# Performance work log

Hardware: AMD Instinct MI355X
Metric: run time of the kernel (lower is better)

Reference implementation:

```python
import jax, jax.numpy as jnp
import numpy as np

B = 1024      # number of states
NP = 32       # SVGD particles per state
AD = 20       # act_dim
OD = 64       # obs_dim
H = 256       # critic hidden width
STEPS = 5     # num_svgd_steps
LR = 0.1      # svgd_lr (adaptive_lr disabled)
SP0 = 1.0     # svgd_sigma_p0
ALIM = 1.0    # act_limit


def _q(obs, X, w1, b1, w2, b2, w3, b3):
    h = jnp.concatenate([obs, X], axis=-1)
    h = jax.nn.relu(h @ w1 + b1)
    h = jax.nn.relu(h @ w2 + b2)
    return jnp.squeeze(h @ w3 + b3, -1)


def _rbf(X):
    # X: [B, NP, AD] -> K [B,NP,NP], diff [B,NP,NP,AD], gamma [B,1,1], K_grad [B,NP,NP,AD]
    diff = X[:, :, None, :] - X[:, None, :, :]
    dist_sq = jnp.sum(diff * diff, axis=-1)
    # adaptive bandwidth via median heuristic (adaptive_sig=True)
    med = jnp.median(dist_sq.reshape(dist_sq.shape[0], -1), axis=-1)
    sig_sq = med / (2.0 * jnp.log(NP + 1.0))
    gamma = (1.0 / (2.0 * sig_sq + 1e-8))[:, None, None]
    K = jnp.exp(-gamma * dist_sq)
    K_grad = -2.0 * gamma[..., None] * diff * K[..., None]  # d/dx_i K(x_i, x_j)
    return K, diff, gamma, K_grad


def setup_inputs():
    key = jax.random.key(0)
    ks = jax.random.split(key, 16)
    N = B * NP

    def lin(k, fi, fo):
        return (jax.random.normal(k, (fi, fo), jnp.float32) / np.sqrt(fi)).astype(jnp.float32)

    return {
        "obs": jax.random.normal(ks[0], (N, OD), jnp.float32),
        "a0": jax.random.normal(ks[1], (N, AD), jnp.float32) * np.sqrt(SP0),
        "q1_w1": lin(ks[2], OD + AD, H), "q1_b1": jnp.zeros((H,), jnp.float32),
        "q1_w2": lin(ks[3], H, H),       "q1_b2": jnp.zeros((H,), jnp.float32),
        "q1_w3": lin(ks[4], H, 1),       "q1_b3": jnp.zeros((1,), jnp.float32),
        "q2_w1": lin(ks[5], OD + AD, H), "q2_b1": jnp.zeros((H,), jnp.float32),
        "q2_w2": lin(ks[6], H, H),       "q2_b2": jnp.zeros((H,), jnp.float32),
        "q2_w3": lin(ks[7], H, 1),       "q2_b3": jnp.zeros((1,), jnp.float32),
    }


def reference(obs, a0, q1_w1, q1_b1, q1_w2, q1_b2, q1_w3, q1_b3,
              q2_w1, q2_b1, q2_w2, q2_b2, q2_w3, q2_b3):
    eye = jnp.eye(NP, dtype=a0.dtype)

    def q_min_sum(Xf):
        q1 = _q(obs, Xf, q1_w1, q1_b1, q1_w2, q1_b2, q1_w3, q1_b3)
        q2 = _q(obs, Xf, q2_w1, q2_b1, q2_w2, q2_b2, q2_w3, q2_b3)
        return jnp.sum(jnp.minimum(q1, q2))

    score_fn = jax.grad(q_min_sum)  # autograd score function

    def step(carry, _):
        a, logp = carry
        score = score_fn(a).reshape(-1, NP, AD)                 # [B,NP,AD]
        X = a.reshape(-1, NP, AD)
        K, diff, gamma, Kg = _rbf(X)
        phi = (jnp.einsum('bij,bjd->bid', K, score) + Kg.sum(axis=1)) / NP
        # log-prob correction terms (with_logprob=True)
        term1 = jnp.mean(jnp.sum(Kg * score[:, None, :, :], axis=-1), axis=2)     # [B,NP]
        inner = jnp.sum(jnp.transpose(Kg, (0, 2, 1, 3)) * diff, axis=-1) \
                - AD * (K - eye)
        term2 = -2.0 * gamma[:, :, 0] * jnp.mean(inner, axis=1)                   # [B,NP]
        logp = logp - LR * (term1 + term2)
        a = a + LR * phi.reshape(a.shape)                        # svgd_optim
        return (a, logp), None

    logp0 = jnp.zeros((B, NP), a0.dtype)
    (a, logp_svgd), _ = jax.lax.scan(step, (a0, logp0), None, length=STEPS)

    a_sq = ALIM * jnp.tanh(a)                                    # [B*NP, AD]
    logp_normal = (-AD * 0.5 * jnp.log(2.0 * jnp.pi * SP0)
                   - 0.5 / SP0 * jnp.sum(a0 * a0, axis=-1)).reshape(-1, NP)
    logp_tanh = -jnp.sum(2.0 * (jnp.log(2.0) - a - jax.nn.softplus(-2.0 * a)),
                         axis=-1).reshape(-1, NP)
    logp_a = jnp.mean(logp_normal + logp_svgd + logp_tanh, axis=-1)  # [B]
    return a_sq, logp_a
```

## Files before the change

kernel.cpp:

```cpp
#include <hip/hip_runtime.h>
#include <math.h>

#define NPART 32
#define ADIM  20
#define ODIM  64
#define HID   256
#define NSTEPS 5
#define LRC   0.1f
#define NBLK  512
#define LOG33 3.4965075614664802f

typedef short bf8 __attribute__((ext_vector_type(8)));
typedef float f4  __attribute__((ext_vector_type(4)));

#define OW1T(n) ((n)*24576)
#define OW2T(n) (49152 + (n)*65536)
#define OW2C(n) (180224 + (n)*65536)
#define OW1X(n) (311296 + (n)*8192)
#define OW3B(n) (327680 + (n)*256)
#define WS_ELEMS 328192

__device__ __forceinline__ short f2bf(float x) {
    unsigned u = __float_as_uint(x);
    u += 0x7FFFu + ((u >> 16) & 1u);
    return (short)(u >> 16);
}
__device__ __forceinline__ short f2bfT(float x) {
    return (short)(__float_as_uint(x) >> 16);
}
__device__ __forceinline__ float bf2f(short s) {
    return __uint_as_float(((unsigned)(unsigned short)s) << 16);
}

#define MFMA(a,b,c) __builtin_amdgcn_mfma_f32_16x16x32_bf16((a),(b),(c),0,0,0)

__global__ void prep_weights(const float* __restrict__ w1a, const float* __restrict__ w2a,
                             const float* __restrict__ w3a, const float* __restrict__ w1b,
                             const float* __restrict__ w2b, const float* __restrict__ w3b,
                             unsigned short* __restrict__ ws)
{
    int idx = blockIdx.x * 256 + threadIdx.x;
    if (idx >= WS_ELEMS) return;
    float val;
    if (idx < 49152) {
        int net = idx / 24576, rem = idx % 24576;
        int n = rem / 96, k = rem % 96;
        const float* w1 = net ? w1b : w1a;
        val = (k < 84) ? w1[k*256 + n] : 0.f;
    } else if (idx < 180224) {
        int t2 = idx - 49152; int net = t2 / 65536, rem = t2 % 65536;
        int n = rem / 256, k = rem % 256;
        const float* w2 = net ? w2b : w2a;
        val = w2[k*256 + n];
    } else if (idx < 311296) {
        int t2 = idx - 180224; int net = t2 / 65536, rem = t2 % 65536;
        const float* w2 = net ? w2b : w2a;
        val = w2[rem];
    } else if (idx < 327680) {
        int t2 = idx - 311296; int net = t2 / 8192, rem = t2 % 8192;
        int d = rem / 256, n = rem % 256;
        const float* w1 = net ? w1b : w1a;
        val = (d < 20) ? w1[(64 + d)*256 + n] : 0.f;
    } else {
        int t2 = idx - 327680; int net = t2 / 256, k = t2 % 256;
        const float* w3 = net ? w3b : w3a;
        val = w3[k];
    }
    ws[idx] = (unsigned short)f2bf(val);
}

__global__ void __launch_bounds__(512, 4)
svgd_main(const float* __restrict__ obs,  const float* __restrict__ a0g,
          const float* __restrict__ b1a,  const float* __restrict__ b2a, const float* __restrict__ b3a,
          const float* __restrict__ b1b,  const float* __restrict__ b2b, const float* __restrict__ b3b,
          const float* __restrict__ w3af, const float* __restrict__ w3bf,
          const unsigned short* __restrict__ ws, float* __restrict__ out)
{
    __shared__ __align__(16) short A0s[64*96];
    __shared__ __align__(16) short hbuf[64*264];
    __shared__ unsigned maskS[2][2][64][8];
    __shared__ float Xm[64*20];
    __shared__ float scoreS[64*21];
    __shared__ float qpart[2][8][64];
    __shared__ int   winsS[64];
    __shared__ float logps[64];
    __shared__ unsigned short lutI[496], lutJ[496];
    __shared__ float med2[4];
    __shared__ float qvS[64];
    __shared__ float normsS[64], diagS[64], rowKS[64];

    float* d2sF = (float*)hbuf;
    float* GSF  = ((float*)hbuf) + 2048;
    short* KbS  = hbuf + 8192;
    short* SBs  = hbuf + 10240;
    short* STbS = hbuf + 12288;
    short* XTbS = hbuf + 14336;

    const int t = threadIdx.x, b = blockIdx.x;
    const int lane = t & 63, wv = t >> 6;
    const int q = lane >> 4, mp = lane & 15;
    const int nb = wv * 32;

    for (int p = t; p < 64*ODIM; p += 512) {
        int i = p >> 6, d = p & 63;
        A0s[i*96 + d] = f2bfT(obs[(b*64 + i)*ODIM + d]);
    }
    for (int p = t; p < 64*ADIM; p += 512) {
        int i = p / 20, d = p - i*20;
        float v = a0g[(b*64 + i)*20 + d];
        Xm[p] = v;
        A0s[i*96 + 64 + d] = f2bfT(v);
    }
    for (int p = t; p < 64*12; p += 512) { int i = p/12, d = p - i*12; A0s[i*96 + 84 + d] = 0; }
    { unsigned* mz = &maskS[0][0][0][0];
      for (int p = t; p < 2*2*64*8; p += 512) mz[p] = 0u; }
    if (t < 496) {
        int i_ = 0, rem = t;
        while (rem >= 31 - i_) { rem -= 31 - i_; ++i_; }
        lutI[t] = (unsigned short)i_; lutJ[t] = (unsigned short)(i_ + 1 + rem);
    }
    if (t < 64) logps[t] = 0.f;
    __syncthreads();

    for (int step = 0; step < NSTEPS; ++step) {
        for (int net = 0; net < 2; ++net) {
            const unsigned short* w1t = ws + OW1T(net);
            const unsigned short* w2t = ws + OW2T(net);
            const float* b1p = net ? b1b : b1a;
            const float* b2p = net ? b2b : b2a;
            const float* w3p = net ? w3bf : w3af;

            f4 acc[4][2];
            #pragma unroll
            for (int h = 0; h < 4; ++h) { acc[h][0] = (f4){0,0,0,0}; acc[h][1] = (f4){0,0,0,0}; }
            {
                const unsigned short* bp0 = w1t + (size_t)(nb +      mp)*96 + q*8;
                const unsigned short* bp1 = w1t + (size_t)(nb + 16 + mp)*96 + q*8;
                bf8 bb0 = *(const bf8*)bp0, bb1 = *(const bf8*)bp1;
                #pragma unroll
                for (int k0 = 0; k0 < 96; k0 += 32) {
                    bf8 n0 = bb0, n1 = bb1;
                    if (k0 + 32 < 96) { n0 = *(const bf8*)(bp0 + k0 + 32); n1 = *(const bf8*)(bp1 + k0 + 32); }
                    #pragma unroll
                    for (int h = 0; h < 4; ++h) {
                        bf8 aa = *(const bf8*)&A0s[(h*16 + mp)*96 + k0 + q*8];
                        acc[h][0] = MFMA(aa, bb0, acc[h][0]);
                        acc[h][1] = MFMA(aa, bb1, acc[h][1]);
                    }
                    bb0 = n0; bb1 = n1;
                }
            }
            #pragma unroll
            for (int h = 0; h < 4; ++h) {
                #pragma unroll
                for (int s = 0; s < 2; ++s) {
                    int n0 = nb + s*16, col = n0 + mp;
                    float bias = b1p[col];
                    #pragma unroll
                    for (int r = 0; r < 4; ++r) {
                        float v = acc[h][s][r] + bias;
                        bool pos = v > 0.f;
                        unsigned long long bal = __ballot(pos);
                        hbuf[(h*16 + q*4 + r)*264 + col] = f2bfT(pos ? v : 0.f);
                        if (mp == 0)
                            atomicOr(&maskS[net][0][h*16 + q*4 + r][n0 >> 5],
                                     ((unsigned)((bal >> (q*16)) & 0xFFFFull)) << (n0 & 16));
                    }
                }
            }
            __syncthreads();

            #pragma unroll
            for (int h = 0; h < 4; ++h) { acc[h][0] = (f4){0,0,0,0}; acc[h][1] = (f4){0,0,0,0}; }
            {
                const unsigned short* bp0 = w2t + (size_t)(nb +      mp)*256 + q*8;
                const unsigned short* bp1 = w2t + (size_t)(nb + 16 + mp)*256 + q*8;
                bf8 bb0 = *(const bf8*)bp0, bb1 = *(const bf8*)bp1;
                #pragma unroll
                for (int k0 = 0; k0 < 256; k0 += 32) {
                    bf8 n0 = bb0, n1 = bb1;
                    if (k0 + 32 < 256) { n0 = *(const bf8*)(bp0 + k0 + 32); n1 = *(const bf8*)(bp1 + k0 + 32); }
                    #pragma unroll
                    for (int h = 0; h < 4; ++h) {
                        bf8 aa = *(const bf8*)&hbuf[(h*16 + mp)*264 + k0 + q*8];
                        acc[h][0] = MFMA(aa, bb0, acc[h][0]);
                        acc[h][1] = MFMA(aa, bb1, acc[h][1]);
                    }
                    bb0 = n0; bb1 = n1;
                }
            }
            {
                float qp[4][4] = {{0,0,0,0},{0,0,0,0},{0,0,0,0},{0,0,0,0}};
                #pragma unroll
                for (int h = 0; h < 4; ++h) {
                    #pragma unroll
                    for (int s = 0; s < 2; ++s) {
                        int n0 = nb + s*16, col = n0 + mp;
                        float bias = b2p[col], w3v = w3p[col];
                        #pragma unroll
                        for (int r = 0; r < 4; ++r) {
                            float v = acc[h][s][r] + bias;
                            bool pos = v > 0.f;
                            unsigned long long bal = __ballot(pos);
                            if (mp == 0)
                                atomicOr(&maskS[net][1][h*16 + q*4 + r][n0 >> 5],
                                         ((unsigned)((bal >> (q*16)) & 0xFFFFull)) << (n0 & 16));
                            qp[h][r] += pos ? v * w3v : 0.f;
                        }
                    }
                }
                #pragma unroll
                for (int d = 1; d < 16; d <<= 1)
                    #pragma unroll
                    for (int h = 0; h < 4; ++h)
                        #pragma unroll
                        for (int r = 0; r < 4; ++r)
                            qp[h][r] += __shfl_xor(qp[h][r], d, 64);
                if (mp == 0) {
                    #pragma unroll
                    for (int h = 0; h < 4; ++h)
                        #pragma unroll
                        for (int r = 0; r < 4; ++r)
                            qpart[net][wv][h*16 + q*4 + r] = qp[h][r];
                }
            }
            __syncthreads();
        }

        if (t < 64) {
            float q0 = b3a[0], q1 = b3b[0];
            #pragma unroll
            for (int w = 0; w < 8; ++w) { q0 += qpart[0][w][t]; q1 += qpart[1][w][t]; }
            winsS[t] = (q0 <= q1) ? 0 : 1;
        }
        __syncthreads();

        for (int net = 0; net < 2; ++net) {
            const unsigned short* w2c  = ws + OW2C(net);
            const unsigned short* w3b8 = ws + OW3B(net);

            f4 acc[4][2];
            #pragma unroll
            for (int h = 0; h < 4; ++h) { acc[h][0] = (f4){0,0,0,0}; acc[h][1] = (f4){0,0,0,0}; }
            int win[4];
            #pragma unroll
            for (int h = 0; h < 4; ++h) win[h] = (winsS[h*16 + mp] == net);
            {
                const unsigned short* bp0 = w2c + (size_t)(nb +      mp)*256 + q*8;
                const unsigned short* bp1 = w2c + (size_t)(nb + 16 + mp)*256 + q*8;
                bf8 bb0 = *(const bf8*)bp0, bb1 = *(const bf8*)bp1;
                #pragma unroll
                for (int k0 = 0; k0 < 256; k0 += 32) {
                    bf8 n0 = bb0, n1 = bb1;
                    if (k0 + 32 < 256) { n0 = *(const bf8*)(bp0 + k0 + 32); n1 = *(const bf8*)(bp1 + k0 + 32); }
                    bf8 w3v = *(const bf8*)(w3b8 + k0 + q*8);
                    #pragma unroll
                    for (int h = 0; h < 4; ++h) {
                        unsigned bits = win[h] ? ((maskS[net][1][h*16 + mp][k0 >> 5] >> (q*8)) & 0xFFu) : 0u;
                        bf8 aa;
                        #pragma unroll
                        for (int j = 0; j < 8; ++j)
                            aa[j] = ((bits >> j) & 1u) ? w3v[j] : (short)0;
                        acc[h][0] = MFMA(aa, bb0, acc[h][0]);
                        acc[h][1] = MFMA(aa, bb1, acc[h][1]);
                    }
                    bb0 = n0; bb1 = n1;
                }
            }
            #pragma unroll
            for (int h = 0; h < 4; ++h) {
                #pragma unroll
                for (int s = 0; s < 2; ++s) {
                    int col = nb + s*16 + mp;
                    #pragma unroll
                    for (int r = 0; r < 4; ++r) {
                        int row = h*16 + q*4 + r;
                        bool on = (maskS[net][0][row][col >> 5] >> (col & 31)) & 1u;
                        hbuf[row*264 + col] = f2bfT(on ? acc[h][s][r] : 0.f);
                    }
                }
            }
            __syncthreads();
            {
                int mt = wv & 3, ch = wv >> 2;
                const unsigned short* w1x = ws + OW1X(net);
                const unsigned short* bp  = w1x + (size_t)(ch*16 + mp)*256 + q*8;
                f4 sa = (f4){0,0,0,0};
                bf8 bx = *(const bf8*)bp;
                #pragma unroll
                for (int k0 = 0; k0 < 256; k0 += 32) {
                    bf8 nx = bx;
                    if (k0 + 32 < 256) nx = *(const bf8*)(bp + k0 + 32);
                    bf8 aa = *(const bf8*)&hbuf[(mt*16 + mp)*264 + k0 + q*8];
                    sa = MFMA(aa, bx, sa);
                    bx = nx;
                }
                int colD = ch*16 + mp;
                if (colD < 20) {
                    #pragma unroll
                    for (int r = 0; r < 4; ++r) {
                        int row = mt*16 + q*4 + r;
                        if (net == 0) scoreS[row*21 + colD]  = sa[r];
                        else          scoreS[row*21 + colD] += sa[r];
                    }
                }
            }
            __syncthreads();
        }

        if (t < 64) {
            int st = t >> 5;
            float nrm = 0.f, dg = 0.f;
            #pragma unroll
            for (int d = 0; d < 20; ++d) {
                float xb = bf2f(A0s[t*96 + 64 + d]);
                nrm += xb * xb;
                float sv = scoreS[t*21 + d];
                float xv = Xm[t*20 + d];
                dg += xv * sv;
                short sb = f2bfT(sv);
                SBs[t*32 + d] = sb;
                STbS[st*1024 + d*32 + (t & 31)] = sb;
                XTbS[st*1024 + d*32 + (t & 31)] = f2bfT(xv);
            }
            #pragma unroll
            for (int d = 20; d < 32; ++d) SBs[t*32 + d] = 0;
            normsS[t] = nrm;
            diagS[t]  = dg;
        }
        __syncthreads();

        {
            int stw = wv >> 2, mt = (wv >> 1) & 1, nt = wv & 1;
            bf8 aa  = *(const bf8*)&A0s[(stw*32 + mt*16 + mp)*96 + 64 + q*8];
            bf8 bbx = *(const bf8*)&A0s[(stw*32 + nt*16 + mp)*96 + 64 + q*8];
            bf8 bbs = *(const bf8*)&SBs[(stw*32 + nt*16 + mp)*32 + q*8];
            f4 gx = MFMA(aa, bbx, ((f4){0,0,0,0}));
            f4 gs = MFMA(aa, bbs, ((f4){0,0,0,0}));
            int jl = nt*16 + mp;
            float nj = normsS[stw*32 + jl];
            #pragma unroll
            for (int r = 0; r < 4; ++r) {
                int il = mt*16 + q*4 + r;
                d2sF[stw*1024 + il*32 + jl] = normsS[stw*32 + il] + nj - 2.f*gx[r];
                GSF [stw*1024 + il*32 + jl] = gs[r];
            }
        }
        __syncthreads();

        if (wv < 2) {
            const float* base = d2sF + wv*1024;
            float v[8];
            #pragma unroll
            for (int i = 0; i < 8; ++i) {
                int e = lane*8 + i;
                v[i] = (e < 496) ? base[lutI[e]*32 + lutJ[e]] : 3.4e38f;
            }
            for (int k = 2; k <= 512; k <<= 1) {
                for (int jj = k >> 1; jj >= 8; jj >>= 1) {
                    int lm = jj >> 3;
                    #pragma unroll
                    for (int i = 0; i < 8; ++i) {
                        float w = __shfl_xor(v[i], lm, 64);
                        int p = lane*8 + i;
                        bool takeMin = (((p & k) == 0) == ((p & jj) == 0));
                        v[i] = takeMin ? fminf(v[i], w) : fmaxf(v[i], w);
                    }
                }
                int jj0 = (k >> 1) < 4 ? (k >> 1) : 4;
                for (int jj = jj0; jj >= 1; jj >>= 1) {
                    #pragma unroll
                    for (int i = 0; i < 8; ++i) {
                        if ((i & jj) == 0) {
                            int i2 = i | jj;
                            int p = lane*8 + i;
                            bool up = ((p & k) == 0);
                            float x = v[i], y = v[i2];
                            float mn = fminf(x, y), mx = fmaxf(x, y);
                            v[i] = up ? mn : mx; v[i2] = up ? mx : mn;
                        }
                    }
                }
            }
            if (lane == 29) med2[wv*2 + 0] = v[7];
            if (lane == 30) med2[wv*2 + 1] = v[0];
        } else {
            unsigned* mz = &maskS[0][0][0][0];
            for (int p = t - 128; p < 2*2*64*8; p += 384) mz[p] = 0u;
        }
        __syncthreads();

        {
            int i = t >> 3, stw = i >> 5, il = i & 31, j0 = (t & 7) * 4;
            float medv = 0.5f * (med2[stw*2] + med2[stw*2 + 1]);
            float gam  = 1.f / (2.f * (medv / (2.f * LOG33)) + 1e-8f);
            float sK = 0.f, sKGS = 0.f, sKd2 = 0.f, sKdg = 0.f;
            #pragma unroll
            for (int jj = 0; jj < 4; ++jj) {
                int j = j0 + jj;
                float d2 = d2sF[stw*1024 + il*32 + j];
                float K  = expf(-gam * d2);
                KbS[stw*1024 + il*32 + j] = f2bfT(K);
                sK   += K;
                sKGS += K * GSF[stw*1024 + il*32 + j];
                sKd2 += K * d2;
                sKdg += K * diagS[stw*32 + j];
            }
            #pragma unroll
            for (int d = 1; d < 8; d <<= 1) {
                sK   += __shfl_xor(sK,   d, 64);
                sKGS += __shfl_xor(sKGS, d, 64);
                sKd2 += __shfl_xor(sKd2, d, 64);
                sKdg += __shfl_xor(sKdg, d, 64);
            }
            if ((t & 7) == 0) {
                rowKS[i] = sK;
                float sdots = sKGS - sKdg;
                float ssum  = -2.f*gam*sdots
                              - 2.f*gam*(2.f*gam*sKd2 - 20.f*(sK - 1.f));
                logps[i] -= LRC * (ssum * (1.f/32.f));
            }
        }
        __syncthreads();

        {
            int stw = wv >> 2, mt = (wv >> 1) & 1, nt = wv & 1;
            float medv = 0.5f * (med2[stw*2] + med2[stw*2 + 1]);
            float gam  = 1.f / (2.f * (medv / (2.f * LOG33)) + 1e-8f);
            bf8 aa  = *(const bf8*)&KbS [stw*1024 + (mt*16 + mp)*32 + q*8];
            bf8 b1v = *(const bf8*)&STbS[stw*1024 + (nt*16 + mp)*32 + q*8];
            bf8 b2v = *(const bf8*)&XTbS[stw*1024 + (nt*16 + mp)*32 + q*8];
            f4 ks = MFMA(aa, b1v, ((f4){0,0,0,0}));
            f4 kx = MFMA(aa, b2v, ((f4){0,0,0,0}));
            int dd = nt*16 + mp;
            if (dd < 20) {
                #pragma unroll
                for (int r = 0; r < 4; ++r) {
                    int gi = stw*32 + mt*16 + q*4 + r;
                    float xi  = Xm[gi*20 + dd];
                    float phi = (ks[r] + 2.f*gam*(xi*rowKS[gi] - kx[r])) * (1.f/32.f);
                    float nx  = xi + LRC * phi;
                    Xm[gi*20 + dd] = nx;
                    A0s[gi*96 + 64 + dd] = f2bfT(nx);
                }
            }
        }
        __syncthreads();
    }

    for (int p = t; p < 64*20; p += 512) {
        int i = p / 20, d = p - i*20;
        out[(b*64 + i)*20 + d] = tanhf(Xm[p]);
    }
    if (t < 64) {
        float lt = 0.f, s0 = 0.f;
        for (int d = 0; d < 20; ++d) {
            float a  = Xm[t*20 + d];
            float x  = -2.f * a;
            float sp = fmaxf(x, 0.f) + log1pf(expf(-fabsf(x)));
            lt -= 2.f * (0.69314718056f - a - sp);
            float v = a0g[(b*64 + t)*20 + d];
            s0 += v * v;
        }
        qvS[t] = -18.3787706641f - 0.5f*s0 + logps[t] + lt;
    }
    __syncthreads();
    if (t < 2) {
        float s = 0.f;
        for (int i = 0; i < 32; ++i) s += qvS[t*32 + i];
        out[1024*32*20 + b*2 + t] = s * (1.f/32.f);
    }
}

extern "C" void kernel_launch(void* const* d_in, const int* in_sizes, int n_in,
                              void* d_out, int out_size, void* d_ws, size_t ws_size,
                              hipStream_t stream) {
    unsigned short* ws = (unsigned short*)d_ws;
    prep_weights<<<(WS_ELEMS + 255)/256, 256, 0, stream>>>(
        (const float*)d_in[2],  (const float*)d_in[4],  (const float*)d_in[6],
        (const float*)d_in[8],  (const float*)d_in[10], (const float*)d_in[12], ws);
    svgd_main<<<NBLK, 512, 0, stream>>>(
        (const float*)d_in[0],  (const float*)d_in[1],
        (const float*)d_in[3],  (const float*)d_in[5],  (const float*)d_in[7],
        (const float*)d_in[9],  (const float*)d_in[11], (const float*)d_in[13],
        (const float*)d_in[6],  (const float*)d_in[12],
        ws, (float*)d_out);
}
```

Before: 497.5 us.

## Interleave twin-critic forward and backward GEMMs to cut barriers and serialization

Unrolls the two-network loops and interleaves independent work. Net-1 layer-1 runs alongside net-0 layer-2, and net-0's backward GEMM runs alongside net-1 layer-2. The winner mask is now applied at the hidden-gradient stage instead of zeroing the weight operand. Score is accumulated in registers and written straight to bf16 buffers, and the diagonal term is read from the GS Gram matrix instead of a separate dot product. This removes several __syncthreads and the scoreS buffer, at the cost of more live accumulators and register pressure, and backward GEMMs now run for both nets on every row.

```diff
diff --git a/kernel.cpp b/kernel.cpp
--- a/kernel.cpp
+++ b/kernel.cpp
@@ -80,14 +80,13 @@
     __shared__ __align__(16) short hbuf[64*264];
     __shared__ unsigned maskS[2][2][64][8];
     __shared__ float Xm[64*20];
-    __shared__ float scoreS[64*21];
     __shared__ float qpart[2][8][64];
     __shared__ int   winsS[64];
     __shared__ float logps[64];
     __shared__ unsigned short lutI[496], lutJ[496];
     __shared__ float med2[4];
     __shared__ float qvS[64];
-    __shared__ float normsS[64], diagS[64], rowKS[64];
+    __shared__ float normsS[64], rowKS[64];
 
     float* d2sF = (float*)hbuf;
     float* GSF  = ((float*)hbuf) + 2048;
@@ -123,31 +122,20 @@
     __syncthreads();
 
     for (int step = 0; step < NSTEPS; ++step) {
-        for (int net = 0; net < 2; ++net) {
-            const unsigned short* w1t = ws + OW1T(net);
-            const unsigned short* w2t = ws + OW2T(net);
-            const float* b1p = net ? b1b : b1a;
-            const float* b2p = net ? b2b : b2a;
-            const float* w3p = net ? w3bf : w3af;
-
+        {
+            const unsigned short* w1t = ws + OW1T(0);
             f4 acc[4][2];
             #pragma unroll
             for (int h = 0; h < 4; ++h) { acc[h][0] = (f4){0,0,0,0}; acc[h][1] = (f4){0,0,0,0}; }
-            {
-                const unsigned short* bp0 = w1t + (size_t)(nb +      mp)*96 + q*8;
-                const unsigned short* bp1 = w1t + (size_t)(nb + 16 + mp)*96 + q*8;
-                bf8 bb0 = *(const bf8*)bp0, bb1 = *(const bf8*)bp1;
-                #pragma unroll
-                for (int k0 = 0; k0 < 96; k0 += 32) {
-                    bf8 n0 = bb0, n1 = bb1;
-                    if (k0 + 32 < 96) { n0 = *(const bf8*)(bp0 + k0 + 32); n1 = *(const bf8*)(bp1 + k0 + 32); }
-                    #pragma unroll
-                    for (int h = 0; h < 4; ++h) {
-                        bf8 aa = *(const bf8*)&A0s[(h*16 + mp)*96 + k0 + q*8];
-                        acc[h][0] = MFMA(aa, bb0, acc[h][0]);
-                        acc[h][1] = MFMA(aa, bb1, acc[h][1]);
-                    }
-                    bb0 = n0; bb1 = n1;
+            #pragma unroll
+            for (int k0 = 0; k0 < 96; k0 += 32) {
+                bf8 bb0 = *(const bf8*)(w1t + (size_t)(nb +      mp)*96 + k0 + q*8);
+                bf8 bb1 = *(const bf8*)(w1t + (size_t)(nb + 16 + mp)*96 + k0 + q*8);
+                #pragma unroll
+                for (int h = 0; h < 4; ++h) {
+                    bf8 aa = *(const bf8*)&A0s[(h*16 + mp)*96 + k0 + q*8];
+                    acc[h][0] = MFMA(aa, bb0, acc[h][0]);
+                    acc[h][1] = MFMA(aa, bb1, acc[h][1]);
                 }
             }
             #pragma unroll
@@ -155,7 +143,7 @@
                 #pragma unroll
                 for (int s = 0; s < 2; ++s) {
                     int n0 = nb + s*16, col = n0 + mp;
-                    float bias = b1p[col];
+                    float bias = b1a[col];
                     #pragma unroll
                     for (int r = 0; r < 4; ++r) {
                         float v = acc[h][s][r] + bias;
@@ -163,69 +151,172 @@
                         unsigned long long bal = __ballot(pos);
                         hbuf[(h*16 + q*4 + r)*264 + col] = f2bfT(pos ? v : 0.f);
                         if (mp == 0)
-                            atomicOr(&maskS[net][0][h*16 + q*4 + r][n0 >> 5],
+                            atomicOr(&maskS[0][0][h*16 + q*4 + r][n0 >> 5],
                                      ((unsigned)((bal >> (q*16)) & 0xFFFFull)) << (n0 & 16));
                     }
                 }
             }
-            __syncthreads();
-
-            #pragma unroll
-            for (int h = 0; h < 4; ++h) { acc[h][0] = (f4){0,0,0,0}; acc[h][1] = (f4){0,0,0,0}; }
-            {
-                const unsigned short* bp0 = w2t + (size_t)(nb +      mp)*256 + q*8;
-                const unsigned short* bp1 = w2t + (size_t)(nb + 16 + mp)*256 + q*8;
-                bf8 bb0 = *(const bf8*)bp0, bb1 = *(const bf8*)bp1;
-                #pragma unroll
-                for (int k0 = 0; k0 < 256; k0 += 32) {
-                    bf8 n0 = bb0, n1 = bb1;
-                    if (k0 + 32 < 256) { n0 = *(const bf8*)(bp0 + k0 + 32); n1 = *(const bf8*)(bp1 + k0 + 32); }
+        }
+        __syncthreads();
+
+        f4 accL2[4][2], accL1[4][2];
+        #pragma unroll
+        for (int h = 0; h < 4; ++h) {
+            accL2[h][0] = (f4){0,0,0,0}; accL2[h][1] = (f4){0,0,0,0};
+            accL1[h][0] = (f4){0,0,0,0}; accL1[h][1] = (f4){0,0,0,0};
+        }
+        {
+            const unsigned short* w2t = ws + OW2T(0);
+            const unsigned short* w1t = ws + OW1T(1);
+            #pragma unroll
+            for (int k0 = 0; k0 < 256; k0 += 32) {
+                bf8 b20 = *(const bf8*)(w2t + (size_t)(nb +      mp)*256 + k0 + q*8);
+                bf8 b21 = *(const bf8*)(w2t + (size_t)(nb + 16 + mp)*256 + k0 + q*8);
+                #pragma unroll
+                for (int h = 0; h < 4; ++h) {
+                    bf8 aa = *(const bf8*)&hbuf[(h*16 + mp)*264 + k0 + q*8];
+                    accL2[h][0] = MFMA(aa, b20, accL2[h][0]);
+                    accL2[h][1] = MFMA(aa, b21, accL2[h][1]);
+                }
+                if (k0 < 96) {
+                    bf8 c0 = *(const bf8*)(w1t + (size_t)(nb +      mp)*96 + k0 + q*8);
+                    bf8 c1 = *(const bf8*)(w1t + (size_t)(nb + 16 + mp)*96 + k0 + q*8);
                     #pragma unroll
                     for (int h = 0; h < 4; ++h) {
-                        bf8 aa = *(const bf8*)&hbuf[(h*16 + mp)*264 + k0 + q*8];
-                        acc[h][0] = MFMA(aa, bb0, acc[h][0]);
-                        acc[h][1] = MFMA(aa, bb1, acc[h][1]);
+                        bf8 aa = *(const bf8*)&A0s[(h*16 + mp)*96 + k0 + q*8];
+                        accL1[h][0] = MFMA(aa, c0, accL1[h][0]);
+                        accL1[h][1] = MFMA(aa, c1, accL1[h][1]);
                     }
-                    bb0 = n0; bb1 = n1;
-                }
-            }
-            {
-                float qp[4][4] = {{0,0,0,0},{0,0,0,0},{0,0,0,0},{0,0,0,0}};
+                }
+            }
+        }
+        {
+            float qp[4][4] = {{0,0,0,0},{0,0,0,0},{0,0,0,0},{0,0,0,0}};
+            #pragma unroll
+            for (int h = 0; h < 4; ++h) {
+                #pragma unroll
+                for (int s = 0; s < 2; ++s) {
+                    int n0 = nb + s*16, col = n0 + mp;
+                    float bias = b2a[col], w3v = w3af[col];
+                    #pragma unroll
+                    for (int r = 0; r < 4; ++r) {
+                        float v = accL2[h][s][r] + bias;
+                        bool pos = v > 0.f;
+                        unsigned long long bal = __ballot(pos);
+                        if (mp == 0)
+                            atomicOr(&maskS[0][1][h*16 + q*4 + r][n0 >> 5],
+                                     ((unsigned)((bal >> (q*16)) & 0xFFFFull)) << (n0 & 16));
+                        qp[h][r] += pos ? v * w3v : 0.f;
+                    }
+                }
+            }
+            #pragma unroll
+            for (int d = 1; d < 16; d <<= 1)
+                #pragma unroll
+                for (int h = 0; h < 4; ++h)
+                    #pragma unroll
+                    for (int r = 0; r < 4; ++r)
+                        qp[h][r] += __shfl_xor(qp[h][r], d, 64);
+            if (mp == 0) {
+                #pragma unroll
+                for (int h = 0; h < 4; ++h)
+                    #pragma unroll
+                    for (int r = 0; r < 4; ++r)
+                        qpart[0][wv][h*16 + q*4 + r] = qp[h][r];
+            }
+        }
+        __syncthreads();
+        #pragma unroll
+        for (int h = 0; h < 4; ++h) {
+            #pragma unroll
+            for (int s = 0; s < 2; ++s) {
+                int n0 = nb + s*16, col = n0 + mp;
+                float bias = b1b[col];
+                #pragma unroll
+                for (int r = 0; r < 4; ++r) {
+                    float v = accL1[h][s][r] + bias;
+                    bool pos = v > 0.f;
+                    unsigned long long bal = __ballot(pos);
+                    hbuf[(h*16 + q*4 + r)*264 + col] = f2bfT(pos ? v : 0.f);
+                    if (mp == 0)
+                        atomicOr(&maskS[1][0][h*16 + q*4 + r][n0 >> 5],
+                                 ((unsigned)((bal >> (q*16)) & 0xFFFFull)) << (n0 & 16));
+                }
+            }
+        }
+        __syncthreads();
+
+        f4 accB0[4][2];
+        #pragma unroll
+        for (int h = 0; h < 4; ++h) {
+            accL2[h][0] = (f4){0,0,0,0}; accL2[h][1] = (f4){0,0,0,0};
+            accB0[h][0] = (f4){0,0,0,0}; accB0[h][1] = (f4){0,0,0,0};
+        }
+        {
+            const unsigned short* w2t  = ws + OW2T(1);
+            const unsigned short* w2c  = ws + OW2C(0);
+            const unsigned short* w3b8 = ws + OW3B(0);
+            #pragma unroll
+            for (int k0 = 0; k0 < 256; k0 += 32) {
+                bf8 b20 = *(const bf8*)(w2t + (size_t)(nb +      mp)*256 + k0 + q*8);
+                bf8 b21 = *(const bf8*)(w2t + (size_t)(nb + 16 + mp)*256 + k0 + q*8);
                 #pragma unroll
                 for (int h = 0; h < 4; ++h) {
-                    #pragma unroll
-                    for (int s = 0; s < 2; ++s) {
-                        int n0 = nb + s*16, col = n0 + mp;
-                        float bias = b2p[col], w3v = w3p[col];
-                        #pragma unroll
-                        for (int r = 0; r < 4; ++r) {
-                            float v = acc[h][s][r] + bias;
-                            bool pos = v > 0.f;
-                            unsigned long long bal = __ballot(pos);
-                            if (mp == 0)
-                                atomicOr(&maskS[net][1][h*16 + q*4 + r][n0 >> 5],
-                                         ((unsigned)((bal >> (q*16)) & 0xFFFFull)) << (n0 & 16));
-                            qp[h][r] += pos ? v * w3v : 0.f;
-                        }
+                    bf8 aa = *(const bf8*)&hbuf[(h*16 + mp)*264 + k0 + q*8];
+                    accL2[h][0] = MFMA(aa, b20, accL2[h][0]);
+                    accL2[h][1] = MFMA(aa, b21, accL2[h][1]);
+                }
+                bf8 c0 = *(const bf8*)(w2c + (size_t)(nb +      mp)*256 + k0 + q*8);
+                bf8 c1 = *(const bf8*)(w2c + (size_t)(nb + 16 + mp)*256 + k0 + q*8);
+                bf8 w3v = *(const bf8*)(w3b8 + k0 + q*8);
+                #pragma unroll
+                for (int h = 0; h < 4; ++h) {
+                    unsigned bits = (maskS[0][1][h*16 + mp][k0 >> 5] >> (q*8)) & 0xFFu;
+                    bf8 aa;
+                    #pragma unroll
+                    for (int j = 0; j < 8; ++j)
+                        aa[j] = ((bits >> j) & 1u) ? w3v[j] : (short)0;
+                    accB0[h][0] = MFMA(aa, c0, accB0[h][0]);
+                    accB0[h][1] = MFMA(aa, c1, accB0[h][1]);
+                }
+            }
+        }
+        {
+            float qp[4][4] = {{0,0,0,0},{0,0,0,0},{0,0,0,0},{0,0,0,0}};
+            #pragma unroll
+            for (int h = 0; h < 4; ++h) {
+                #pragma unroll
+                for (int s = 0; s < 2; ++s) {
+                    int n0 = nb + s*16, col = n0 + mp;
+                    float bias = b2b[col], w3v = w3bf[col];
+                    #pragma unroll
+                    for (int r = 0; r < 4; ++r) {
+                        float v = accL2[h][s][r] + bias;
+                        bool pos = v > 0.f;
+                        unsigned long long bal = __ballot(pos);
+                        if (mp == 0)
+                            atomicOr(&maskS[1][1][h*16 + q*4 + r][n0 >> 5],
+                                     ((unsigned)((bal >> (q*16)) & 0xFFFFull)) << (n0 & 16));
+                        qp[h][r] += pos ? v * w3v : 0.f;
                     }
                 }
-                #pragma unroll
-                for (int d = 1; d < 16; d <<= 1)
-                    #pragma unroll
-                    for (int h = 0; h < 4; ++h)
-                        #pragma unroll
-                        for (int r = 0; r < 4; ++r)
-                            qp[h][r] += __shfl_xor(qp[h][r], d, 64);
-                if (mp == 0) {
-                    #pragma unroll
-                    for (int h = 0; h < 4; ++h)
-                        #pragma unroll
-                        for (int r = 0; r < 4; ++r)
-                            qpart[net][wv][h*16 + q*4 + r] = qp[h][r];
-                }
-            }
-            __syncthreads();
-        }
+            }
+            #pragma unroll
+            for (int d = 1; d < 16; d <<= 1)
+                #pragma unroll
+                for (int h = 0; h < 4; ++h)
+                    #pragma unroll
+                    for (int r = 0; r < 4; ++r)
+                        qp[h][r] += __shfl_xor(qp[h][r], d, 64);
+            if (mp == 0) {
+                #pragma unroll
+                for (int h = 0; h < 4; ++h)
+                    #pragma unroll
+                    for (int r = 0; r < 4; ++r)
+                        qpart[1][wv][h*16 + q*4 + r] = qp[h][r];
+            }
+        }
+        __syncthreads();
 
         if (t < 64) {
             float q0 = b3a[0], q1 = b3b[0];
@@ -233,115 +324,123 @@
             for (int w = 0; w < 8; ++w) { q0 += qpart[0][w][t]; q1 += qpart[1][w][t]; }
             winsS[t] = (q0 <= q1) ? 0 : 1;
         }
-        __syncthreads();
-
-        for (int net = 0; net < 2; ++net) {
-            const unsigned short* w2c  = ws + OW2C(net);
-            const unsigned short* w3b8 = ws + OW3B(net);
-
-            f4 acc[4][2];
-            #pragma unroll
-            for (int h = 0; h < 4; ++h) { acc[h][0] = (f4){0,0,0,0}; acc[h][1] = (f4){0,0,0,0}; }
-            int win[4];
-            #pragma unroll
-            for (int h = 0; h < 4; ++h) win[h] = (winsS[h*16 + mp] == net);
-            {
-                const unsigned short* bp0 = w2c + (size_t)(nb +      mp)*256 + q*8;
-                const unsigned short* bp1 = w2c + (size_t)(nb + 16 + mp)*256 + q*8;
-                bf8 bb0 = *(const bf8*)bp0, bb1 = *(const bf8*)bp1;
-                #pragma unroll
-                for (int k0 = 0; k0 < 256; k0 += 32) {
-                    bf8 n0 = bb0, n1 = bb1;
-                    if (k0 + 32 < 256) { n0 = *(const bf8*)(bp0 + k0 + 32); n1 = *(const bf8*)(bp1 + k0 + 32); }
-                    bf8 w3v = *(const bf8*)(w3b8 + k0 + q*8);
-                    #pragma unroll
-                    for (int h = 0; h < 4; ++h) {
-                        unsigned bits = win[h] ? ((maskS[net][1][h*16 + mp][k0 >> 5] >> (q*8)) & 0xFFu) : 0u;
-                        bf8 aa;
-                        #pragma unroll
-                        for (int j = 0; j < 8; ++j)
-                            aa[j] = ((bits >> j) & 1u) ? w3v[j] : (short)0;
-                        acc[h][0] = MFMA(aa, bb0, acc[h][0]);
-                        acc[h][1] = MFMA(aa, bb1, acc[h][1]);
-                    }
-                    bb0 = n0; bb1 = n1;
-                }
-            }
-            #pragma unroll
-            for (int h = 0; h < 4; ++h) {
-                #pragma unroll
-                for (int s = 0; s < 2; ++s) {
-                    int col = nb + s*16 + mp;
-                    #pragma unroll
-                    for (int r = 0; r < 4; ++r) {
-                        int row = h*16 + q*4 + r;
-                        bool on = (maskS[net][0][row][col >> 5] >> (col & 31)) & 1u;
-                        hbuf[row*264 + col] = f2bfT(on ? acc[h][s][r] : 0.f);
-                    }
-                }
-            }
-            __syncthreads();
-            {
-                int mt = wv & 3, ch = wv >> 2;
-                const unsigned short* w1x = ws + OW1X(net);
-                const unsigned short* bp  = w1x + (size_t)(ch*16 + mp)*256 + q*8;
-                f4 sa = (f4){0,0,0,0};
-                bf8 bx = *(const bf8*)bp;
-                #pragma unroll
-                for (int k0 = 0; k0 < 256; k0 += 32) {
-                    bf8 nx = bx;
-                    if (k0 + 32 < 256) nx = *(const bf8*)(bp + k0 + 32);
-                    bf8 aa = *(const bf8*)&hbuf[(mt*16 + mp)*264 + k0 + q*8];
-                    sa = MFMA(aa, bx, sa);
-                    bx = nx;
-                }
-                int colD = ch*16 + mp;
-                if (colD < 20) {
-                    #pragma unroll
-                    for (int r = 0; r < 4; ++r) {
-                        int row = mt*16 + q*4 + r;
-                        if (net == 0) scoreS[row*21 + colD]  = sa[r];
-                        else          scoreS[row*21 + colD] += sa[r];
-                    }
-                }
-            }
-            __syncthreads();
-        }
-
+        f4 accB1[4][2];
+        #pragma unroll
+        for (int h = 0; h < 4; ++h) { accB1[h][0] = (f4){0,0,0,0}; accB1[h][1] = (f4){0,0,0,0}; }
+        {
+            const unsigned short* w2c  = ws + OW2C(1);
+            const unsigned short* w3b8 = ws + OW3B(1);
+            #pragma unroll
+            for (int k0 = 0; k0 < 256; k0 += 32) {
+                bf8 c0 = *(const bf8*)(w2c + (size_t)(nb +      mp)*256 + k0 + q*8);
+                bf8 c1 = *(const bf8*)(w2c + (size_t)(nb + 16 + mp)*256 + k0 + q*8);
+                bf8 w3v = *(const bf8*)(w3b8 + k0 + q*8);
+                #pragma unroll
+                for (int h = 0; h < 4; ++h) {
+                    unsigned bits = (maskS[1][1][h*16 + mp][k0 >> 5] >> (q*8)) & 0xFFu;
+                    bf8 aa;
+                    #pragma unroll
+                    for (int j = 0; j < 8; ++j)
+                        aa[j] = ((bits >> j) & 1u) ? w3v[j] : (short)0;
+                    accB1[h][0] = MFMA(aa, c0, accB1[h][0]);
+                    accB1[h][1] = MFMA(aa, c1, accB1[h][1]);
+                }
+            }
+        }
+        __syncthreads();
+        #pragma unroll
+        for (int h = 0; h < 4; ++h) {
+            #pragma unroll
+            for (int s = 0; s < 2; ++s) {
+                int col = nb + s*16 + mp;
+                #pragma unroll
+                for (int r = 0; r < 4; ++r) {
+                    int row = h*16 + q*4 + r;
+                    bool on = (winsS[row] == 0) &&
+                              ((maskS[0][0][row][col >> 5] >> (col & 31)) & 1u);
+                    hbuf[row*264 + col] = f2bfT(on ? accB0[h][s][r] : 0.f);
+                }
+            }
+        }
+        __syncthreads();
+
+        const int mt = wv & 3, ch = wv >> 2;
+        f4 sa0 = (f4){0,0,0,0};
+        {
+            const unsigned short* w1x = ws + OW1X(0);
+            #pragma unroll
+            for (int k0 = 0; k0 < 256; k0 += 32) {
+                bf8 bx = *(const bf8*)(w1x + (size_t)(ch*16 + mp)*256 + k0 + q*8);
+                bf8 aa = *(const bf8*)&hbuf[(mt*16 + mp)*264 + k0 + q*8];
+                sa0 = MFMA(aa, bx, sa0);
+            }
+        }
+        __syncthreads();
+        #pragma unroll
+        for (int h = 0; h < 4; ++h) {
+            #pragma unroll
+            for (int s = 0; s < 2; ++s) {
+                int col = nb + s*16 + mp;
+                #pragma unroll
+                for (int r = 0; r < 4; ++r) {
+                    int row = h*16 + q*4 + r;
+                    bool on = (winsS[row] == 1) &&
+                              ((maskS[1][0][row][col >> 5] >> (col & 31)) & 1u);
+                    hbuf[row*264 + col] = f2bfT(on ? accB1[h][s][r] : 0.f);
+                }
+            }
+        }
+        __syncthreads();
+
+        f4 sa = sa0;
+        {
+            const unsigned short* w1x = ws + OW1X(1);
+            #pragma unroll
+            for (int k0 = 0; k0 < 256; k0 += 32) {
+                bf8 bx = *(const bf8*)(w1x + (size_t)(ch*16 + mp)*256 + k0 + q*8);
+                bf8 aa = *(const bf8*)&hbuf[(mt*16 + mp)*264 + k0 + q*8];
+                sa = MFMA(aa, bx, sa);
+            }
+        }
+        __syncthreads();
+
+        {
+            int colD = ch*16 + mp;
+            #pragma unroll
+            for (int r = 0; r < 4; ++r) {
+                int row = mt*16 + q*4 + r, st = row >> 5, il = row & 31;
+                short sb = f2bfT(sa[r]);
+                SBs[row*32 + colD] = sb;
+                STbS[st*1024 + colD*32 + il] = sb;
+            }
+        }
         if (t < 64) {
-            int st = t >> 5;
-            float nrm = 0.f, dg = 0.f;
+            int st = t >> 5, il = t & 31;
+            float nrm = 0.f;
             #pragma unroll
             for (int d = 0; d < 20; ++d) {
                 float xb = bf2f(A0s[t*96 + 64 + d]);
                 nrm += xb * xb;
-                float sv = scoreS[t*21 + d];
-                float xv = Xm[t*20 + d];
-                dg += xv * sv;
-                short sb = f2bfT(sv);
-                SBs[t*32 + d] = sb;
-                STbS[st*1024 + d*32 + (t & 31)] = sb;
-                XTbS[st*1024 + d*32 + (t & 31)] = f2bfT(xv);
-            }
-            #pragma unroll
-            for (int d = 20; d < 32; ++d) SBs[t*32 + d] = 0;
+                XTbS[st*1024 + d*32 + il] = f2bfT(Xm[t*20 + d]);
+            }
+            #pragma unroll
+            for (int d = 20; d < 32; ++d) XTbS[st*1024 + d*32 + il] = 0;
             normsS[t] = nrm;
-            diagS[t]  = dg;
-        }
-        __syncthreads();
-
-        {
-            int stw = wv >> 2, mt = (wv >> 1) & 1, nt = wv & 1;
-            bf8 aa  = *(const bf8*)&A0s[(stw*32 + mt*16 + mp)*96 + 64 + q*8];
-            bf8 bbx = *(const bf8*)&A0s[(stw*32 + nt*16 + mp)*96 + 64 + q*8];
-            bf8 bbs = *(const bf8*)&SBs[(stw*32 + nt*16 + mp)*32 + q*8];
+        }
+        __syncthreads();
+
+        {
+            int stw = wv >> 2, mtl = (wv >> 1) & 1, ntl = wv & 1;
+            bf8 aa  = *(const bf8*)&A0s[(stw*32 + mtl*16 + mp)*96 + 64 + q*8];
+            bf8 bbx = *(const bf8*)&A0s[(stw*32 + ntl*16 + mp)*96 + 64 + q*8];
+            bf8 bbs = *(const bf8*)&SBs[(stw*32 + ntl*16 + mp)*32 + q*8];
             f4 gx = MFMA(aa, bbx, ((f4){0,0,0,0}));
             f4 gs = MFMA(aa, bbs, ((f4){0,0,0,0}));
-            int jl = nt*16 + mp;
+            int jl = ntl*16 + mp;
             float nj = normsS[stw*32 + jl];
             #pragma unroll
             for (int r = 0; r < 4; ++r) {
-                int il = mt*16 + q*4 + r;
+                int il = mtl*16 + q*4 + r;
                 d2sF[stw*1024 + il*32 + jl] = normsS[stw*32 + il] + nj - 2.f*gx[r];
                 GSF [stw*1024 + il*32 + jl] = gs[r];
             }
@@ -404,7 +503,7 @@
                 sK   += K;
                 sKGS += K * GSF[stw*1024 + il*32 + j];
                 sKd2 += K * d2;
-                sKdg += K * diagS[stw*32 + j];
+                sKdg += K * GSF[stw*1024 + j*32 + j];
             }
             #pragma unroll
             for (int d = 1; d < 8; d <<= 1) {
@@ -424,19 +523,19 @@
         __syncthreads();
 
         {
-            int stw = wv >> 2, mt = (wv >> 1) & 1, nt = wv & 1;
+            int stw = wv >> 2, mtl = (wv >> 1) & 1, ntl = wv & 1;
             float medv = 0.5f * (med2[stw*2] + med2[stw*2 + 1]);
             float gam  = 1.f / (2.f * (medv / (2.f * LOG33)) + 1e-8f);
-            bf8 aa  = *(const bf8*)&KbS [stw*1024 + (mt*16 + mp)*32 + q*8];
-            bf8 b1v = *(const bf8*)&STbS[stw*1024 + (nt*16 + mp)*32 + q*8];
-            bf8 b2v = *(const bf8*)&XTbS[stw*1024 + (nt*16 + mp)*32 + q*8];
+            bf8 aa  = *(const bf8*)&KbS [stw*1024 + (mtl*16 + mp)*32 + q*8];
+            bf8 b1v = *(const bf8*)&STbS[stw*1024 + (ntl*16 + mp)*32 + q*8];
+            bf8 b2v = *(const bf8*)&XTbS[stw*1024 + (ntl*16 + mp)*32 + q*8];
             f4 ks = MFMA(aa, b1v, ((f4){0,0,0,0}));
             f4 kx = MFMA(aa, b2v, ((f4){0,0,0,0}));
-            int dd = nt*16 + mp;
+            int dd = ntl*16 + mp;
             if (dd < 20) {
                 #pragma unroll
                 for (int r = 0; r < 4; ++r) {
-                    int gi = stw*32 + mt*16 + q*4 + r;
+                    int gi = stw*32 + mtl*16 + q*4 + r;
                     float xi  = Xm[gi*20 + dd];
                     float phi = (ks[r] + 2.f*gam*(xi*rowKS[gi] - kx[r])) * (1.f/32.f);
                     float nx  = xi + LRC * phi;
```

Result: slower. 1.308 ms (+162.9%).
